# Performance work log

Measured on AMD Instinct MI355X. Metric: run time of the kernel, lower is better.

Reference implementation:

```python
import jax, jax.numpy as jnp
import numpy as np

N = 100000   # num_nodes_total
E = 1600000  # num edges (avg degree 16)
ES = 30000   # scored triples
R = 16       # num_relations
D = 128      # cfg.dim


def setup_inputs() -> dict:
    key = jax.random.key(0)
    ks = jax.random.split(key, 10)
    x0 = 0.01 * jax.random.normal(ks[0], (N, D), dtype=jnp.float32)  # Embedding init std=0.01
    # GCNConv lin: Glorot init, no bias in lin; separate zero bias added post-aggregation
    glorot = np.sqrt(6.0 / (D + D)).astype(np.float32)
    W1 = jax.random.uniform(ks[1], (D, D), jnp.float32, -glorot, glorot)
    b1 = jnp.zeros((D,), jnp.float32)
    W2 = jax.random.uniform(ks[2], (D, D), jnp.float32, -glorot, glorot)
    b2 = jnp.zeros((D,), jnp.float32)
    rel_W = jax.random.uniform(ks[3], (R, D, D), jnp.float32, -glorot, glorot)  # xavier_uniform
    edge_index = jax.random.randint(ks[4], (2, E), 0, N)
    rel_ids = jax.random.randint(ks[5], (ES,), 0, R)
    head = jax.random.randint(ks[6], (ES,), 0, N)
    tail = jax.random.randint(ks[7], (ES,), 0, N)
    return {"x0": x0, "W1": W1, "b1": b1, "W2": W2, "b2": b2,
            "rel_W": rel_W, "edge_index": edge_index, "rel_ids": rel_ids,
            "head": head, "tail": tail}


def _gcn_conv(x, W, b, src, dst, norm):
    # GCNConv(add_self_loops=False, normalize=True): out = scatter(norm * (xW)[src] -> dst) + b
    h = x @ W                           # (N, D)
    msg = h[src] * norm[:, None]        # (E, D)
    return jax.ops.segment_sum(msg, dst, num_segments=x.shape[0]) + b


def reference(x0, W1, b1, W2, b2, rel_W, edge_index, rel_ids, head, tail):
    src, dst = edge_index[0], edge_index[1]
    n = x0.shape[0]
    # symmetric gcn_norm without self-loops: deg over targets, norm = d^-1/2[src]*d^-1/2[dst]
    deg = jax.ops.segment_sum(jnp.ones_like(src, dtype=x0.dtype), dst, num_segments=n)
    dinv = jnp.where(deg > 0, 1.0 / jnp.sqrt(jnp.maximum(deg, 1.0)), 0.0)
    norm = dinv[src] * dinv[dst]
    # encode (eval mode: dropout is identity)
    x = jax.nn.relu(_gcn_conv(x0, W1, b1, src, dst, norm))
    z = _gcn_conv(x, W2, b2, src, dst, norm)
    # score_logits_all_rel: z[head]^T W[rel] z[tail]
    scores = jnp.einsum('ed,edf,ef->e', z[head], rel_W[rel_ids], z[tail])
    return scores
```

## Files before the change

kernel.cpp:

```cpp
#include <hip/hip_runtime.h>
#include <hip/hip_bf16.h>

#define TD 128
#define WS 136
#define SC_T 8
#define BKT_SH 7
#define NBLK 256

typedef __attribute__((ext_vector_type(8))) short bf16x8;
typedef __attribute__((ext_vector_type(4))) float f32x4;

static __device__ __forceinline__ unsigned short f2bf(float f) {
    unsigned int u = __float_as_uint(f);
    u += 0x7fffu + ((u >> 16) & 1u);
    return (unsigned short)(u >> 16);
}
static __device__ __forceinline__ float bf2f(unsigned short h) {
    return __uint_as_float((unsigned int)h << 16);
}


__global__ __launch_bounds__(256) void kc_hist(const int* __restrict__ ei, int* __restrict__ bh,
                                               const int* __restrict__ rel, int* __restrict__ rcount,
                                               int E_, int ES_, int NB, int chunk, int rchunk) {
    __shared__ int lh[1024];
    __shared__ int rh[16];
    int t = threadIdx.x, blk = blockIdx.x;
    for (int j = t; j < NB; j += 256) lh[j] = 0;
    if (t < 16) rh[t] = 0;
    __syncthreads();
    int e0 = blk * chunk, e1 = min(E_, e0 + chunk);
    for (int e = e0 + t; e < e1; e += 256)
        atomicAdd(&lh[ei[E_ + e] >> BKT_SH], 1);
    int r0 = blk * rchunk, r1 = min(ES_, r0 + rchunk);
    for (int e = r0 + t; e < r1; e += 256)
        atomicAdd(&rh[rel[e]], 1);
    __syncthreads();
    for (int j = t; j < NB; j += 256) bh[(size_t)j * NBLK + blk] = lh[j];
    if (t < 16 && rh[t]) atomicAdd(&rcount[t], rh[t]);
}

__global__ __launch_bounds__(64) void kc_scanA(int* __restrict__ bh, int* __restrict__ tot, int NB) {
    int b = blockIdx.x, l = threadIdx.x;
    int* row = bh + (size_t)b * NBLK;
    int run = 0;
#pragma unroll
    for (int g = 0; g < NBLK / 64; ++g) {
        int v = row[g * 64 + l];
        int x = v;
#pragma unroll
        for (int off = 1; off < 64; off <<= 1) {
            int y = __shfl_up(x, off);
            if (l >= off) x += y;
        }
        row[g * 64 + l] = run + x - v;
        run += __shfl(x, 63);
    }
    if (l == 0) tot[b] = run;
}

__global__ __launch_bounds__(256) void kc_scanB(const int* __restrict__ tot, int* __restrict__ boff,
                                                int NB, int* __restrict__ rowptrN) {
    __shared__ int wsum[4];
    int t = threadIdx.x;
    int base = t * 4;
    int a0 = (base     < NB) ? tot[base]     : 0;
    int a1 = (base + 1 < NB) ? tot[base + 1] : 0;
    int a2 = (base + 2 < NB) ? tot[base + 2] : 0;
    int a3 = (base + 3 < NB) ? tot[base + 3] : 0;
    int s1 = a0 + a1, s2 = s1 + a2, tt = s2 + a3;
    int lane = t & 63, wv = t >> 6;
    int x = tt;
#pragma unroll
    for (int off = 1; off < 64; off <<= 1) {
        int y = __shfl_up(x, off);
        if (lane >= off) x += y;
    }
    if (lane == 63) wsum[wv] = x;
    __syncthreads();
    int woff = 0;
    for (int w = 0; w < wv; ++w) woff += wsum[w];
    int excl = woff + x - tt;
    if (base     < NB) boff[base]     = excl;
    if (base + 1 < NB) boff[base + 1] = excl + a0;
    if (base + 2 < NB) boff[base + 2] = excl + s1;
    if (base + 3 < NB) boff[base + 3] = excl + s2;
    if (t == 255) { boff[NB] = woff + x; *rowptrN = woff + x; }
}

__global__ __launch_bounds__(256) void kc_scat(const int* __restrict__ ei, const int* __restrict__ bh,
                                               const int* __restrict__ boff, int* __restrict__ ebuf,
                                               int E_, int NB, int chunk) {
    __shared__ int lh[1024];
    int t = threadIdx.x, blk = blockIdx.x;
    for (int j = t; j < NB; j += 256) lh[j] = 0;
    __syncthreads();
    int e0 = blk * chunk, e1 = min(E_, e0 + chunk);
    for (int e = e0 + t; e < e1; e += 256) {
        int s = ei[e];
        int d = ei[E_ + e];
        int b = d >> BKT_SH;
        int lr = atomicAdd(&lh[b], 1);
        int slot = boff[b] + bh[(size_t)b * NBLK + blk] + lr;
        ebuf[slot] = (s << BKT_SH) | (d & ((1 << BKT_SH) - 1));
    }
}

__global__ __launch_bounds__(256) void kc_build(const int* __restrict__ ebuf, const int* __restrict__ boff,
                                                int* __restrict__ rowptr, float* __restrict__ dinv,
                                                int* __restrict__ esrc, int n) {
    __shared__ int hist[128], excl[128], cur[128];
    __shared__ int w0;
    int b = blockIdx.x, t = threadIdx.x;
    int node0 = b << BKT_SH;
    int s = boff[b], e = boff[b + 1];
    if (t < 128) { hist[t] = 0; cur[t] = 0; }
    __syncthreads();
    for (int i = s + t; i < e; i += 256)
        atomicAdd(&hist[ebuf[i] & 127], 1);
    __syncthreads();
    int v = (t < 128) ? hist[t] : 0;
    int lane = t & 63, wv = t >> 6;
    int x = v;
#pragma unroll
    for (int off = 1; off < 64; off <<= 1) {
        int y = __shfl_up(x, off);
        if (lane >= off) x += y;
    }
    if (t == 63) w0 = x;
    __syncthreads();
    if (t < 128) {
        int ex = x - v + (wv == 1 ? w0 : 0);
        excl[t] = ex;
        int node = node0 + t;
        if (node < n) {
            rowptr[node] = s + ex;
            dinv[node] = (v > 0) ? 1.0f / sqrtf((float)v) : 0.0f;
        }
    }
    __syncthreads();
    for (int i = s + t; i < e; i += 256) {
        int p = ebuf[i];
        int loc = p & 127;
        int lr = atomicAdd(&cur[loc], 1);
        esrc[s + excl[loc] + lr] = p >> BKT_SH;
    }
}

__global__ __launch_bounds__(256) void k_wsplit(const float* __restrict__ W1, const float* __restrict__ W2,
                                                unsigned short* __restrict__ Wt) {
    int i = blockIdx.x * 256 + threadIdx.x;
    int w = i >> 14;
    int idx = i & 16383;
    int k = idx >> 7, n = idx & 127;
    float x = (w ? W2 : W1)[idx];
    unsigned short h = f2bf(x);
    unsigned short l = f2bf(x - bf2f(h));
    size_t base = (size_t)w * 32768;
    Wt[base + n * 128 + k] = h;
    Wt[base + 16384 + n * 128 + k] = l;
}

__global__ __launch_bounds__(256, 2) void k_gemm(const float* __restrict__ X,
                                                 const unsigned short* __restrict__ Wth,
                                                 const unsigned short* __restrict__ Wtl,
                                                 const float* __restrict__ scale,
                                                 unsigned short* __restrict__ out,
                                                 int nrows) {
    __shared__ __align__(16) unsigned short Wl[2][128 * WS];
    const int t = threadIdx.x;
    const int w = t >> 6;
    const int lane = t & 63;
    const int l15 = lane & 15;
    const int quad = lane >> 4;
    const int rbase = blockIdx.x * 64 + w * 16;
    const int arow = rbase + l15;
    const bool avalid = arow < nrows;

    float4 xa[4][2];
#pragma unroll
    for (int kc = 0; kc < 4; ++kc) {
        const float* src = X + (size_t)arow * TD + kc * 32 + quad * 8;
        xa[kc][0] = avalid ? *(const float4*)src       : make_float4(0.f, 0.f, 0.f, 0.f);
        xa[kc][1] = avalid ? *(const float4*)(src + 4) : make_float4(0.f, 0.f, 0.f, 0.f);
    }

    {
        const uint4* gh = (const uint4*)Wth;
        const uint4* gl = (const uint4*)Wtl;
#pragma unroll
        for (int it = 0; it < 8; ++it) {
            int idx = t + it * 256;
            int n = idx >> 4, kg = idx & 15;
            uint4 vh = gh[idx];
            uint4 vl = gl[idx];
            *(uint4*)&Wl[0][n * WS + kg * 8] = vh;
            *(uint4*)&Wl[1][n * WS + kg * 8] = vl;
        }
    }

    bf16x8 ah[4], al[4];
#pragma unroll
    for (int kc = 0; kc < 4; ++kc) {
#pragma unroll
        for (int j = 0; j < 8; ++j) {
            float v = (j < 4) ? ((const float*)&xa[kc][0])[j] : ((const float*)&xa[kc][1])[j - 4];
            unsigned short h = f2bf(v);
            ah[kc][j] = (short)h;
            al[kc][j] = (short)f2bf(v - bf2f(h));
        }
    }
    __syncthreads();

    f32x4 acc[8];
#pragma unroll
    for (int b = 0; b < 8; ++b) acc[b] = (f32x4){0.f, 0.f, 0.f, 0.f};

#pragma unroll
    for (int kc = 0; kc < 4; ++kc) {
        const int koff = kc * 32 + quad * 8;
#pragma unroll
        for (int b = 0; b < 8; ++b) {
            const int boff = (b * 16 + l15) * WS + koff;
            bf16x8 bh = *(const bf16x8*)&Wl[0][boff];
            bf16x8 bl = *(const bf16x8*)&Wl[1][boff];
            acc[b] = __builtin_amdgcn_mfma_f32_16x16x32_bf16(ah[kc], bh, acc[b], 0, 0, 0);
            acc[b] = __builtin_amdgcn_mfma_f32_16x16x32_bf16(al[kc], bh, acc[b], 0, 0, 0);
            acc[b] = __builtin_amdgcn_mfma_f32_16x16x32_bf16(ah[kc], bl, acc[b], 0, 0, 0);
        }
    }

    {
        int grow = rbase + quad * 4;
        if (grow < nrows) {
            float4 s4 = *(const float4*)&scale[grow];
#pragma unroll
            for (int b = 0; b < 8; ++b) {
                int col = b * 16 + l15;
                out[(size_t)(grow + 0) * TD + col] = f2bf(acc[b][0] * s4.x);
                out[(size_t)(grow + 1) * TD + col] = f2bf(acc[b][1] * s4.y);
                out[(size_t)(grow + 2) * TD + col] = f2bf(acc[b][2] * s4.z);
                out[(size_t)(grow + 3) * TD + col] = f2bf(acc[b][3] * s4.w);
            }
        }
    }
}

#define ACC8(p, u) \
    p##0 += __uint_as_float(u.x << 16); p##1 += __uint_as_float(u.x & 0xffff0000u); \
    p##2 += __uint_as_float(u.y << 16); p##3 += __uint_as_float(u.y & 0xffff0000u); \
    p##4 += __uint_as_float(u.z << 16); p##5 += __uint_as_float(u.z & 0xffff0000u); \
    p##6 += __uint_as_float(u.w << 16); p##7 += __uint_as_float(u.w & 0xffff0000u);

__global__ __launch_bounds__(256) void k_agg(const unsigned short* __restrict__ hs, const int* __restrict__ rowptr,
                                             const int* __restrict__ esrc, const float* __restrict__ dinv,
                                             const float* __restrict__ bias, float* __restrict__ out,
                                             int n, int relu) {
    int node = blockIdx.x * 16 + (threadIdx.x >> 4);
    int lane = threadIdx.x & 15;
    if (node >= n) return;
    int s = rowptr[node], e = rowptr[node + 1];
    const uint4* h16 = (const uint4*)hs;
    float a0 = 0.f, a1 = 0.f, a2 = 0.f, a3 = 0.f, a4 = 0.f, a5 = 0.f, a6 = 0.f, a7 = 0.f;
    float c0 = 0.f, c1 = 0.f, c2 = 0.f, c3 = 0.f, c4 = 0.f, c5 = 0.f, c6 = 0.f, c7 = 0.f;
    int i = s;
    for (; i + 4 <= e; i += 4) {
        int s0 = esrc[i], s1 = esrc[i + 1], s2 = esrc[i + 2], s3 = esrc[i + 3];
        uint4 u0 = h16[(size_t)s0 * 16 + lane];
        uint4 u1 = h16[(size_t)s1 * 16 + lane];
        uint4 u2 = h16[(size_t)s2 * 16 + lane];
        uint4 u3 = h16[(size_t)s3 * 16 + lane];
        ACC8(a, u0)
        ACC8(c, u1)
        ACC8(a, u2)
        ACC8(c, u3)
    }
    for (; i < e; ++i) {
        uint4 u = h16[(size_t)esrc[i] * 16 + lane];
        ACC8(a, u)
    }
    a0 += c0; a1 += c1; a2 += c2; a3 += c3;
    a4 += c4; a5 += c5; a6 += c6; a7 += c7;
    float di = dinv[node];
    float4 b0 = ((const float4*)bias)[lane * 2];
    float4 b1 = ((const float4*)bias)[lane * 2 + 1];
    float o0 = fmaf(di, a0, b0.x);
    float o1 = fmaf(di, a1, b0.y);
    float o2 = fmaf(di, a2, b0.z);
    float o3 = fmaf(di, a3, b0.w);
    float o4 = fmaf(di, a4, b1.x);
    float o5 = fmaf(di, a5, b1.y);
    float o6 = fmaf(di, a6, b1.z);
    float o7 = fmaf(di, a7, b1.w);
    if (relu) {
        o0 = fmaxf(o0, 0.f); o1 = fmaxf(o1, 0.f); o2 = fmaxf(o2, 0.f); o3 = fmaxf(o3, 0.f);
        o4 = fmaxf(o4, 0.f); o5 = fmaxf(o5, 0.f); o6 = fmaxf(o6, 0.f); o7 = fmaxf(o7, 0.f);
    }
    ((float4*)out)[(size_t)node * 32 + lane * 2]     = make_float4(o0, o1, o2, o3);
    ((float4*)out)[(size_t)node * 32 + lane * 2 + 1] = make_float4(o4, o5, o6, o7);
}

__global__ void k_roff(const int* __restrict__ rcount, int* __restrict__ roff,
                       int* __restrict__ chunkoff, int* __restrict__ cursor, int nr) {
    if (threadIdx.x == 0 && blockIdx.x == 0) {
        int run = 0, crun = 0;
        for (int r = 0; r < nr; ++r) {
            roff[r] = run; chunkoff[r] = crun; cursor[r] = run;
            run += rcount[r]; crun += (rcount[r] + SC_T - 1) / SC_T;
        }
        roff[nr] = run; chunkoff[nr] = crun;
    }
}

__global__ __launch_bounds__(256) void k_bucket(const int* __restrict__ rel, int* __restrict__ cursor,
                                                int* __restrict__ eidx, int es) {
    __shared__ int lh[16];
    __shared__ int lbase[16];
    int t = threadIdx.x;
    if (t < 16) lh[t] = 0;
    __syncthreads();
    int r[4], lr[4];
#pragma unroll
    for (int i = 0; i < 4; ++i) {
        int e = blockIdx.x * 1024 + i * 256 + t;
        if (e < es) {
            r[i] = rel[e];
            lr[i] = atomicAdd(&lh[r[i]], 1);
        } else r[i] = -1;
    }
    __syncthreads();
    if (t < 16) lbase[t] = lh[t] ? atomicAdd(&cursor[t], lh[t]) : 0;
    __syncthreads();
#pragma unroll
    for (int i = 0; i < 4; ++i)
        if (r[i] >= 0) eidx[lbase[r[i]] + lr[i]] = blockIdx.x * 1024 + i * 256 + t;
}

__global__ __launch_bounds__(256) void k_score_r(const float* __restrict__ z, const float* __restrict__ relW,
                                                 const int* __restrict__ eidx, const int* __restrict__ head,
                                                 const int* __restrict__ tail, const int* __restrict__ roff,
                                                 const int* __restrict__ chunkoff, float* __restrict__ out,
                                                 int R_, int cpb) {
    __shared__ __align__(16) float Wl[TD * TD];
    __shared__ __align__(16) float zhL[SC_T * TD];
    __shared__ __align__(16) float ztL[SC_T * TD];
    __shared__ int eids[SC_T];
    __shared__ int co[17], ro[17];
    __shared__ float red[4][SC_T];
    const int t = threadIdx.x;
    if (t < 17 && t <= R_) { co[t] = chunkoff[t]; ro[t] = roff[t]; }
    __syncthreads();
    const int nch = co[R_];
    int b = blockIdx.x * cpb;
    const int bend = min(nch, b + cpb);
    int r = 0, rprev = -1;
    for (; b < bend; ++b) {
        while (co[r + 1] <= b) ++r;
        const int base = ro[r] + (b - co[r]) * SC_T;
        const int nt = min(SC_T, ro[r + 1] - base);
        if (t < SC_T) eids[t] = (t < nt) ? eidx[base + t] : -1;
        const bool newW = (r != rprev);
        rprev = r;
        __syncthreads();
        {
            int tt = t >> 5, c4 = t & 31;
            float4 vh = make_float4(0.f, 0.f, 0.f, 0.f), vt = vh;
            int e = eids[tt];
            if (e >= 0) {
                vh = ((const float4*)(z + (size_t)head[e] * TD))[c4];
                vt = ((const float4*)(z + (size_t)tail[e] * TD))[c4];
            }
            ((float4*)(zhL + tt * TD))[c4] = vh;
            ((float4*)(ztL + tt * TD))[c4] = vt;
        }
        if (newW) {
            const float4* W4 = (const float4*)(relW + (size_t)r * TD * TD);
            float4* Wl4 = (float4*)Wl;
#pragma unroll
            for (int i = 0; i < 16; ++i) Wl4[t + i * 256] = W4[t + i * 256];
        }
        __syncthreads();

        const int c  = (t & 31) * 4;
        const int i0 = (t >> 5) * 16;
        float4 acc[SC_T];
#pragma unroll
        for (int u = 0; u < SC_T; ++u) acc[u] = make_float4(0.f, 0.f, 0.f, 0.f);
#pragma unroll 4
        for (int i = i0; i < i0 + 16; ++i) {
            float4 wv = *(const float4*)&Wl[i * TD + c];
#pragma unroll
            for (int u = 0; u < SC_T; ++u) {
                float h = zhL[u * TD + i];
                acc[u].x = fmaf(h, wv.x, acc[u].x);
                acc[u].y = fmaf(h, wv.y, acc[u].y);
                acc[u].z = fmaf(h, wv.z, acc[u].z);
                acc[u].w = fmaf(h, wv.w, acc[u].w);
            }
        }
        float pth[SC_T];
#pragma unroll
        for (int u = 0; u < SC_T; ++u) {
            float4 z4 = *(const float4*)&ztL[u * TD + c];
            pth[u] = acc[u].x * z4.x + acc[u].y * z4.y + acc[u].z * z4.z + acc[u].w * z4.w;
        }
#pragma unroll
        for (int off = 32; off > 0; off >>= 1)
#pragma unroll
            for (int u = 0; u < SC_T; ++u) pth[u] += __shfl_down(pth[u], off);
        if ((t & 63) == 0) {
            int wv = t >> 6;
#pragma unroll
            for (int u = 0; u < SC_T; ++u) red[wv][u] = pth[u];
        }
        __syncthreads();
        if (t < SC_T) {
            int e = eids[t];
            if (e >= 0) out[e] = red[0][t] + red[1][t] + red[2][t] + red[3][t];
        }
    }
}

extern "C" void kernel_launch(void* const* d_in, const int* in_sizes, int n_in,
                              void* d_out, int out_size, void* d_ws, size_t ws_size,
                              hipStream_t stream) {
    const float* x0   = (const float*)d_in[0];
    const float* W1   = (const float*)d_in[1];
    const float* b1   = (const float*)d_in[2];
    const float* W2   = (const float*)d_in[3];
    const float* b2   = (const float*)d_in[4];
    const float* relW = (const float*)d_in[5];
    const int*   ei   = (const int*)d_in[6];
    const int*   rel  = (const int*)d_in[7];
    const int*   head = (const int*)d_in[8];
    const int*   tail = (const int*)d_in[9];
    float* outp = (float*)d_out;

    const int N_  = in_sizes[0] / TD;
    const int E_  = in_sizes[6] / 2;
    const int ES_ = in_sizes[7];
    const int R_  = in_sizes[5] / (TD * TD);
    const int ntiles64 = (N_ + 63) / 64;
    const int NB    = (N_ + (1 << BKT_SH) - 1) >> BKT_SH;
    const int chunk  = (E_ + NBLK - 1) / NBLK;
    const int rchunk = (ES_ + NBLK - 1) / NBLK;
    const int maxch  = (ES_ + SC_T - 1) / SC_T + R_;
    const int sgrid  = maxch < 512 ? maxch : 512;
    const int cpb    = (maxch + sgrid - 1) / sgrid;

    char* p = (char*)d_ws;
    auto alloc = [&](size_t bytes) { char* r = p; p += (bytes + 255) & ~(size_t)255; return r; };
    float*          dinv   = (float*)         alloc((size_t)N_ * 4);
    int*            rowptr = (int*)           alloc(((size_t)N_ + 1) * 4);
    int*            bh     = (int*)           alloc((size_t)NB * NBLK * 4);
    int*            tot    = (int*)           alloc((size_t)NB * 4);
    int*            boff   = (int*)           alloc(((size_t)NB + 1) * 4);
    int*            esrc   = (int*)           alloc((size_t)E_ * 4);
    unsigned short* Wt     = (unsigned short*)alloc((size_t)4 * 16384 * 2);
    int*            rcount = (int*)           alloc((size_t)R_ * 4);
    int*            roff   = (int*)           alloc(((size_t)R_ + 1) * 4);
    int*            chkoff = (int*)           alloc(((size_t)R_ + 1) * 4);
    int*            cursor = (int*)           alloc((size_t)R_ * 4);
    int*            eidx   = (int*)           alloc((size_t)ES_ * 4);
    unsigned short* bufA   = (unsigned short*)alloc((size_t)N_ * TD * 2);
    float*          bufB   = (float*)         alloc((size_t)N_ * TD * 4);
    int*            ebuf   = (int*)bufA;

    hipMemsetAsync(rcount, 0, (size_t)R_ * 4, stream);

    kc_hist <<<NBLK, 256, 0, stream>>>(ei, bh, rel, rcount, E_, ES_, NB, chunk, rchunk);
    kc_scanA<<<NB, 64, 0, stream>>>(bh, tot, NB);
    kc_scanB<<<1, 256, 0, stream>>>(tot, boff, NB, rowptr + N_);
    kc_scat <<<NBLK, 256, 0, stream>>>(ei, bh, boff, ebuf, E_, NB, chunk);
    kc_build<<<NB, 256, 0, stream>>>(ebuf, boff, rowptr, dinv, esrc, N_);

    k_wsplit<<<128, 256, 0, stream>>>(W1, W2, Wt);

    k_roff  <<<1, 64, 0, stream>>>(rcount, roff, chkoff, cursor, R_);
    k_bucket<<<(ES_ + 1023) / 1024, 256, 0, stream>>>(rel, cursor, eidx, ES_);

    k_gemm<<<ntiles64, 256, 0, stream>>>(x0, Wt, Wt + 16384, dinv, bufA, N_);
    k_agg <<<(N_ + 15) / 16, 256, 0, stream>>>(bufA, rowptr, esrc, dinv, b1, bufB, N_, 1);
    k_gemm<<<ntiles64, 256, 0, stream>>>(bufB, Wt + 32768, Wt + 49152, dinv, bufA, N_);
    k_agg <<<(N_ + 15) / 16, 256, 0, stream>>>(bufA, rowptr, esrc, dinv, b2, bufB, N_, 0);

    k_score_r<<<sgrid, 256, 0, stream>>>(bufB, relW, eidx, head, tail,
                                         roff, chkoff, outp, R_, cpb);
}
```

Measured before the change: 356.6 us.

## Quantize GEMM output to per-row int8 for gather-aggregation

The GEMM epilogue now quantizes each scaled output row to int8 with a per-row absmax scale, staging the bytes through LDS for coalesced stores. The aggregation kernel gathers 8-byte int8 chunks plus one per-source scale instead of 16-byte bf16 chunks, halving the bytes moved by the random gathers. This adds quantization error (7-bit mantissa-equivalent per row) that may exceed tolerance, plus extra shuffle and LDS work in the GEMM epilogue.

```diff
diff --git a/kernel.cpp b/kernel.cpp
--- a/kernel.cpp
+++ b/kernel.cpp
@@ -165,7 +165,8 @@
                                                  const unsigned short* __restrict__ Wth,
                                                  const unsigned short* __restrict__ Wtl,
                                                  const float* __restrict__ scale,
-                                                 unsigned short* __restrict__ out,
+                                                 unsigned char* __restrict__ out8,
+                                                 float* __restrict__ scOut,
                                                  int nrows) {
     __shared__ __align__(16) unsigned short Wl[2][128 * WS];
     const int t = threadIdx.x;
@@ -230,54 +231,97 @@
         }
     }
 
+    __syncthreads();
+
     {
-        int grow = rbase + quad * 4;
-        if (grow < nrows) {
-            float4 s4 = *(const float4*)&scale[grow];
+        unsigned char* lds8 = (unsigned char*)&Wl[0][0];
+        const int grow = rbase + quad * 4;
+        float4 s4 = make_float4(0.f, 0.f, 0.f, 0.f);
+        if (grow < nrows) s4 = *(const float4*)&scale[grow];
+        float rm[4];
+#pragma unroll
+        for (int j = 0; j < 4; ++j) {
+            float sj = ((const float*)&s4)[j];
+            float mx = 0.f;
 #pragma unroll
             for (int b = 0; b < 8; ++b) {
-                int col = b * 16 + l15;
-                out[(size_t)(grow + 0) * TD + col] = f2bf(acc[b][0] * s4.x);
-                out[(size_t)(grow + 1) * TD + col] = f2bf(acc[b][1] * s4.y);
-                out[(size_t)(grow + 2) * TD + col] = f2bf(acc[b][2] * s4.z);
-                out[(size_t)(grow + 3) * TD + col] = f2bf(acc[b][3] * s4.w);
+                acc[b][j] *= sj;
+                mx = fmaxf(mx, fabsf(acc[b][j]));
             }
-        }
-    }
-}
-
-#define ACC8(p, u) \
-    p##0 += __uint_as_float(u.x << 16); p##1 += __uint_as_float(u.x & 0xffff0000u); \
-    p##2 += __uint_as_float(u.y << 16); p##3 += __uint_as_float(u.y & 0xffff0000u); \
-    p##4 += __uint_as_float(u.z << 16); p##5 += __uint_as_float(u.z & 0xffff0000u); \
-    p##6 += __uint_as_float(u.w << 16); p##7 += __uint_as_float(u.w & 0xffff0000u);
-
-__global__ __launch_bounds__(256) void k_agg(const unsigned short* __restrict__ hs, const int* __restrict__ rowptr,
-                                             const int* __restrict__ esrc, const float* __restrict__ dinv,
-                                             const float* __restrict__ bias, float* __restrict__ out,
-                                             int n, int relu) {
+            rm[j] = mx;
+        }
+#pragma unroll
+        for (int m_ = 1; m_ < 16; m_ <<= 1)
+#pragma unroll
+            for (int j = 0; j < 4; ++j) rm[j] = fmaxf(rm[j], __shfl_xor(rm[j], m_));
+        float inv[4];
+#pragma unroll
+        for (int j = 0; j < 4; ++j) inv[j] = rm[j] > 0.f ? 127.f / rm[j] : 0.f;
+#pragma unroll
+        for (int j = 0; j < 4; ++j) {
+            int lrow = w * 16 + quad * 4 + j;
+#pragma unroll
+            for (int b = 0; b < 8; ++b) {
+                int q = (int)rintf(acc[b][j] * inv[j]);
+                lds8[lrow * 128 + b * 16 + l15] = (unsigned char)(signed char)q;
+            }
+        }
+        if (l15 == 0 && grow < nrows)
+            *(float4*)&scOut[grow] = make_float4(rm[0] * (1.f / 127.f), rm[1] * (1.f / 127.f),
+                                                 rm[2] * (1.f / 127.f), rm[3] * (1.f / 127.f));
+    }
+    __syncthreads();
+    {
+        const unsigned int* lds32 = (const unsigned int*)&Wl[0][0];
+        unsigned int* g32 = (unsigned int*)out8;
+#pragma unroll
+        for (int k = 0; k < 8; ++k) {
+            int idx = t + k * 256;
+            int row = blockIdx.x * 64 + (idx >> 5);
+            if (row < nrows) g32[(size_t)blockIdx.x * 2048 + idx] = lds32[idx];
+        }
+    }
+}
+
+#define ACCI8(p, u, s) \
+    p##0 = fmaf(s, (float)(signed char)(u.x      ), p##0); \
+    p##1 = fmaf(s, (float)(signed char)(u.x >>  8), p##1); \
+    p##2 = fmaf(s, (float)(signed char)(u.x >> 16), p##2); \
+    p##3 = fmaf(s, (float)(signed char)(u.x >> 24), p##3); \
+    p##4 = fmaf(s, (float)(signed char)(u.y      ), p##4); \
+    p##5 = fmaf(s, (float)(signed char)(u.y >>  8), p##5); \
+    p##6 = fmaf(s, (float)(signed char)(u.y >> 16), p##6); \
+    p##7 = fmaf(s, (float)(signed char)(u.y >> 24), p##7);
+
+__global__ __launch_bounds__(256) void k_agg(const unsigned char* __restrict__ hs8, const float* __restrict__ sc,
+                                             const int* __restrict__ rowptr, const int* __restrict__ esrc,
+                                             const float* __restrict__ dinv, const float* __restrict__ bias,
+                                             float* __restrict__ out, int n, int relu) {
     int node = blockIdx.x * 16 + (threadIdx.x >> 4);
     int lane = threadIdx.x & 15;
     if (node >= n) return;
     int s = rowptr[node], e = rowptr[node + 1];
-    const uint4* h16 = (const uint4*)hs;
+    const uint2* h8 = (const uint2*)hs8;
     float a0 = 0.f, a1 = 0.f, a2 = 0.f, a3 = 0.f, a4 = 0.f, a5 = 0.f, a6 = 0.f, a7 = 0.f;
     float c0 = 0.f, c1 = 0.f, c2 = 0.f, c3 = 0.f, c4 = 0.f, c5 = 0.f, c6 = 0.f, c7 = 0.f;
     int i = s;
     for (; i + 4 <= e; i += 4) {
         int s0 = esrc[i], s1 = esrc[i + 1], s2 = esrc[i + 2], s3 = esrc[i + 3];
-        uint4 u0 = h16[(size_t)s0 * 16 + lane];
-        uint4 u1 = h16[(size_t)s1 * 16 + lane];
-        uint4 u2 = h16[(size_t)s2 * 16 + lane];
-        uint4 u3 = h16[(size_t)s3 * 16 + lane];
-        ACC8(a, u0)
-        ACC8(c, u1)
-        ACC8(a, u2)
-        ACC8(c, u3)
+        uint2 u0 = h8[(size_t)s0 * 16 + lane];
+        uint2 u1 = h8[(size_t)s1 * 16 + lane];
+        uint2 u2 = h8[(size_t)s2 * 16 + lane];
+        uint2 u3 = h8[(size_t)s3 * 16 + lane];
+        float f0 = sc[s0], f1 = sc[s1], f2 = sc[s2], f3 = sc[s3];
+        ACCI8(a, u0, f0)
+        ACCI8(c, u1, f1)
+        ACCI8(a, u2, f2)
+        ACCI8(c, u3, f3)
     }
     for (; i < e; ++i) {
-        uint4 u = h16[(size_t)esrc[i] * 16 + lane];
-        ACC8(a, u)
+        int s0 = esrc[i];
+        uint2 u = h8[(size_t)s0 * 16 + lane];
+        float f = sc[s0];
+        ACCI8(a, u, f)
     }
     a0 += c0; a1 += c1; a2 += c2; a3 += c3;
     a4 += c4; a5 += c5; a6 += c6; a7 += c7;
@@ -462,7 +506,8 @@
     int*            chkoff = (int*)           alloc(((size_t)R_ + 1) * 4);
     int*            cursor = (int*)           alloc((size_t)R_ * 4);
     int*            eidx   = (int*)           alloc((size_t)ES_ * 4);
-    unsigned short* bufA   = (unsigned short*)alloc((size_t)N_ * TD * 2);
+    unsigned char*  bufA   = (unsigned char*) alloc((size_t)N_ * TD);
+    float*          sc     = (float*)         alloc((size_t)N_ * 4);
     float*          bufB   = (float*)         alloc((size_t)N_ * TD * 4);
     int*            ebuf   = (int*)bufA;
 
@@ -479,10 +524,10 @@
     k_roff  <<<1, 64, 0, stream>>>(rcount, roff, chkoff, cursor, R_);
     k_bucket<<<(ES_ + 1023) / 1024, 256, 0, stream>>>(rel, cursor, eidx, ES_);
 
-    k_gemm<<<ntiles64, 256, 0, stream>>>(x0, Wt, Wt + 16384, dinv, bufA, N_);
-    k_agg <<<(N_ + 15) / 16, 256, 0, stream>>>(bufA, rowptr, esrc, dinv, b1, bufB, N_, 1);
-    k_gemm<<<ntiles64, 256, 0, stream>>>(bufB, Wt + 32768, Wt + 49152, dinv, bufA, N_);
-    k_agg <<<(N_ + 15) / 16, 256, 0, stream>>>(bufA, rowptr, esrc, dinv, b2, bufB, N_, 0);
+    k_gemm<<<ntiles64, 256, 0, stream>>>(x0, Wt, Wt + 16384, dinv, bufA, sc, N_);
+    k_agg <<<(N_ + 15) / 16, 256, 0, stream>>>(bufA, sc, rowptr, esrc, dinv, b1, bufB, N_, 1);
+    k_gemm<<<ntiles64, 256, 0, stream>>>(bufB, Wt + 32768, Wt + 49152, dinv, bufA, sc, N_);
+    k_agg <<<(N_ + 15) / 16, 256, 0, stream>>>(bufA, sc, rowptr, esrc, dinv, b2, bufB, N_, 0);
 
     k_score_r<<<sgrid, 256, 0, stream>>>(bufB, relW, eidx, head, tail,
                                          roff, chkoff, outp, R_, cpb);
```

Result: faster. 326.1 us (-8.6%).
